# Optimization experiments

Measured on AMD Instinct MI355X. Metric: run time of the kernel, lower is better.

The kernel has to match this reference:

```python
import jax, jax.numpy as jnp
import numpy as np
from math import sqrt

V, D, H, HD, L, F, P, NL = 32000, 768, 12, 64, 12, 3072, 2048, 2
B, S = 8, 1024
EPS = 1e-5


def setup_inputs() -> dict:
    key = jax.random.key(0)
    ks = jax.random.split(key, 12)
    n = lambda k, sh: (jax.random.normal(k, sh, jnp.float32) * 0.02)
    return {
        'tokens': jax.random.randint(ks[0], (B, S), 0, V, dtype=jnp.int32),
        'tok_emb': n(ks[1], (V, D)),
        'pos_emb': n(ks[2], (P, D)),
        'emb_ln_s': jnp.ones((D,), jnp.float32), 'emb_ln_b': jnp.zeros((D,), jnp.float32),
        'Wq': n(ks[3], (L, H, D, HD)), 'bq': jnp.zeros((L, H, HD), jnp.float32),
        'Wk': n(ks[4], (L, H, D, HD)), 'bk': jnp.zeros((L, H, HD), jnp.float32),
        'Wv': n(ks[5], (L, H, D, HD)), 'bv': jnp.zeros((L, H, HD), jnp.float32),
        'Wo': n(ks[6], (L, D, D)), 'bo': jnp.zeros((L, D), jnp.float32),
        'ln1_s': jnp.ones((L, D), jnp.float32), 'ln1_b': jnp.zeros((L, D), jnp.float32),
        'ln2_s': jnp.ones((L, D), jnp.float32), 'ln2_b': jnp.zeros((L, D), jnp.float32),
        'W1': n(ks[7], (L, D, F)), 'b1': jnp.zeros((L, F), jnp.float32),
        'W2': n(ks[8], (L, F, D)), 'b2': jnp.zeros((L, D), jnp.float32),
        'Wc': n(ks[9], (D, NL)), 'bc': jnp.zeros((NL,), jnp.float32),
    }


def _ln(x, s, b):
    m = jnp.mean(x, -1, keepdims=True)
    v = jnp.mean((x - m) ** 2, -1, keepdims=True)
    return (x - m) * jax.lax.rsqrt(v + EPS) * s + b


def reference(tokens, tok_emb, pos_emb, emb_ln_s, emb_ln_b,
              Wq, bq, Wk, bk, Wv, bv, Wo, bo,
              ln1_s, ln1_b, ln2_s, ln2_b, W1, b1, W2, b2, Wc, bc):
    b, s = tokens.shape
    # embeddings (dropout is eval-mode identity)
    x = tok_emb[tokens] + pos_emb[:s][None, :, :]          # [b, s, D]
    x = _ln(x, emb_ln_s, emb_ln_b)
    scale = 1.0 / sqrt(HD)
    for l in range(L):
        xn = _ln(x, ln1_s[l], ln1_b[l])
        q = jnp.einsum('bsd,hdk->bhsk', xn, Wq[l]) + bq[l][:, None, :]
        k = jnp.einsum('bsd,hdk->bhsk', xn, Wk[l]) + bk[l][:, None, :]
        v = jnp.einsum('bsd,hdk->bhsk', xn, Wv[l]) + bv[l][:, None, :]
        scores = jnp.einsum('bhsk,bhtk->bhst', q, k) * scale   # [b,H,s,s]
        w = jax.nn.softmax(scores, axis=-1)
        o = jnp.einsum('bhst,bhtk->bhsk', w, v)                # [b,H,s,HD]
        o = o.transpose(0, 2, 1, 3).reshape(b, s, D)           # concat heads
        x = x + o @ Wo[l] + bo[l]
        xn = _ln(x, ln2_s[l], ln2_b[l])
        h = jax.nn.gelu(xn @ W1[l] + b1[l], approximate=False)
        x = x + h @ W2[l] + b2[l]
    # CLS token -> classifier (dropout identity)
    return x[:, 0, :] @ Wc + bc                                # [b, NL]
```

## Files before the change

kernel.cpp:

```cpp
#include <hip/hip_runtime.h>
#include <hip/hip_bf16.h>
#include <math.h>

#define B_   8
#define S_   1024
#define D_   768
#define H_   12
#define HD_  64
#define L_   12
#define F_   3072
#define NTOK 8192

typedef __bf16 bf16x8 __attribute__((ext_vector_type(8)));
typedef float  f32x4  __attribute__((ext_vector_type(4)));
typedef unsigned short u16;

static __device__ __forceinline__ unsigned short f2bf_bits(float f) {
    __hip_bfloat16 h = __float2bfloat16(f);
    return __builtin_bit_cast(unsigned short, h);
}
static __device__ __forceinline__ float bf2f(unsigned short u) {
    unsigned int t = ((unsigned int)u) << 16;
    return __builtin_bit_cast(float, t);
}
static __device__ __forceinline__ void gload16(const void* g, void* l) {
    __builtin_amdgcn_global_load_lds(
        (__attribute__((address_space(1))) void*)g,
        (__attribute__((address_space(3))) void*)l, 16, 0, 0);
}

__global__ __launch_bounds__(256)
void prep_layer_kernel(const float* __restrict__ Wq, const float* __restrict__ Wk,
                       const float* __restrict__ Wv, const float* __restrict__ Wo,
                       const float* __restrict__ W1, const float* __restrict__ W2,
                       int l, __hip_bfloat16* __restrict__ wbuf)
{
    const int id = blockIdx.x;
    const float* src; __hip_bfloat16* dst;
    int R, C, r0, c0;
    if (id < 432) {
        int dtile = id % 12, t = id / 12;
        int which = t / 12, h = t % 12;
        src = (which == 0 ? Wq : which == 1 ? Wk : Wv) + (size_t)(l*12 + h) * 768 * 64;
        dst = wbuf + (size_t)(which*768 + h*64) * 768;
        R = 768; C = 64; r0 = dtile * 64; c0 = 0;
    } else if (id < 576) {
        int t = id - 432;
        src = Wo + (size_t)l * 768 * 768;
        dst = wbuf + 1769472;
        R = 768; C = 768; r0 = (t / 12) * 64; c0 = (t % 12) * 64;
    } else if (id < 1152) {
        int t = id - 576;
        src = W1 + (size_t)l * 768 * 3072;
        dst = wbuf + 2359296;
        R = 768; C = 3072; r0 = (t % 12) * 64; c0 = (t / 12) * 64;
    } else {
        int t = id - 1152;
        src = W2 + (size_t)l * 3072 * 768;
        dst = wbuf + 4718592;
        R = 3072; C = 768; r0 = (t / 12) * 64; c0 = (t % 12) * 64;
    }
    __shared__ float tile[64][65];
    for (int i = threadIdx.x; i < 4096; i += 256) {
        int rr = i >> 6, cc = i & 63;
        tile[rr][cc] = src[(size_t)(r0 + rr) * C + (c0 + cc)];
    }
    __syncthreads();
    for (int i = threadIdx.x; i < 4096; i += 256) {
        int cc = i >> 6, rr = i & 63;
        dst[(size_t)(c0 + cc) * R + (r0 + rr)] = __float2bfloat16(tile[rr][cc]);
    }
}

__global__ __launch_bounds__(256)
void prep_bqkv_kernel(const float* __restrict__ bq, const float* __restrict__ bk,
                      const float* __restrict__ bv, float* __restrict__ bqkv)
{
    int i = blockIdx.x * 256 + threadIdx.x;
    int l = i / 2304, c = i % 2304;
    int which = c / 768, hk = c % 768;
    const float* src = which == 0 ? bq : which == 1 ? bk : bv;
    bqkv[i] = src[l*768 + hk];
}

__global__ __launch_bounds__(256)
void embed_ln_kernel(const int* __restrict__ tokens, const float* __restrict__ tok_emb,
                     const float* __restrict__ pos_emb, const float* __restrict__ gam,
                     const float* __restrict__ bet, float* __restrict__ x)
{
    const int row  = blockIdx.x*4 + (threadIdx.x >> 6);
    const int lane = threadIdx.x & 63;
    const int s    = row & (S_-1);
    const int tok  = tokens[row];
    const float* te = tok_emb + (size_t)tok * D_;
    const float* pe = pos_emb + (size_t)s   * D_;
    float v[12]; float s1 = 0.f, s2 = 0.f;
#pragma unroll
    for (int c = 0; c < 3; ++c) {
        const int base = c*256 + lane*4;
        float4 a = *(const float4*)(te + base);
        float4 p = *(const float4*)(pe + base);
        float t0 = a.x+p.x, t1 = a.y+p.y, t2 = a.z+p.z, t3 = a.w+p.w;
        v[c*4+0]=t0; v[c*4+1]=t1; v[c*4+2]=t2; v[c*4+3]=t3;
        s1 += t0+t1+t2+t3;
        s2 += t0*t0 + t1*t1 + t2*t2 + t3*t3;
    }
#pragma unroll
    for (int off = 32; off > 0; off >>= 1) { s1 += __shfl_xor(s1, off); s2 += __shfl_xor(s2, off); }
    const float mean = s1 * (1.f/768.f);
    const float rstd = rsqrtf(s2*(1.f/768.f) - mean*mean + 1e-5f);
    float* xr = x + (size_t)row * D_;
#pragma unroll
    for (int c = 0; c < 3; ++c) {
        const int base = c*256 + lane*4;
        float4 g = *(const float4*)(gam + base);
        float4 bb = *(const float4*)(bet + base);
        float4 o;
        o.x = (v[c*4+0]-mean)*rstd*g.x + bb.x;
        o.y = (v[c*4+1]-mean)*rstd*g.y + bb.y;
        o.z = (v[c*4+2]-mean)*rstd*g.z + bb.z;
        o.w = (v[c*4+3]-mean)*rstd*g.w + bb.w;
        *(float4*)(xr + base) = o;
    }
}

__global__ __launch_bounds__(256)
void ln_kernel(const float* __restrict__ xin, const float* __restrict__ gam,
               const float* __restrict__ bet, __hip_bfloat16* __restrict__ out)
{
    const int row  = blockIdx.x*4 + (threadIdx.x >> 6);
    const int lane = threadIdx.x & 63;
    const float* xr = xin + (size_t)row * D_;
    float v[12]; float s1 = 0.f, s2 = 0.f;
#pragma unroll
    for (int c = 0; c < 3; ++c) {
        float4 t = *(const float4*)(xr + c*256 + lane*4);
        v[c*4+0]=t.x; v[c*4+1]=t.y; v[c*4+2]=t.z; v[c*4+3]=t.w;
        s1 += t.x+t.y+t.z+t.w;
        s2 += t.x*t.x + t.y*t.y + t.z*t.z + t.w*t.w;
    }
#pragma unroll
    for (int off = 32; off > 0; off >>= 1) { s1 += __shfl_xor(s1, off); s2 += __shfl_xor(s2, off); }
    const float mean = s1 * (1.f/768.f);
    const float rstd = rsqrtf(s2*(1.f/768.f) - mean*mean + 1e-5f);
    unsigned short* op = (unsigned short*)out + (size_t)row * D_;
#pragma unroll
    for (int c = 0; c < 3; ++c) {
        const int base = c*256 + lane*4;
        float4 g = *(const float4*)(gam + base);
        float4 bb = *(const float4*)(bet + base);
        ushort4 pk;
        pk.x = f2bf_bits((v[c*4+0]-mean)*rstd*g.x + bb.x);
        pk.y = f2bf_bits((v[c*4+1]-mean)*rstd*g.y + bb.y);
        pk.z = f2bf_bits((v[c*4+2]-mean)*rstd*g.z + bb.z);
        pk.w = f2bf_bits((v[c*4+3]-mean)*rstd*g.w + bb.w);
        *(ushort4*)(op + base) = pk;
    }
}

template<int EPI>
__global__ __launch_bounds__(256)
void gemm_kernel(const __hip_bfloat16* __restrict__ A,
                 const __hip_bfloat16* __restrict__ Bt,
                 const float* __restrict__ bias,
                 __hip_bfloat16* __restrict__ outb,
                 __hip_bfloat16* __restrict__ outv,
                 int N, int K, int nTiles)
{
    __shared__ __hip_bfloat16 As[128*64];
    __shared__ __hip_bfloat16 Bs[128*64];

    const int tid  = threadIdx.x;
    const int lane = tid & 63;
    const int wid  = tid >> 6;

    const int nwg   = gridDim.x;
    const int chunk = nwg >> 3;
    const int bid   = blockIdx.x;
    const int swz   = (bid & 7) * chunk + (bid >> 3);
    const int m0 = (swz / nTiles) * 128;
    const int n0 = (swz % nTiles) * 128;

    const int srow = wid*32 + (lane >> 3);
    const int scol = ((lane & 7) ^ (srow & 7)) * 8;
    const __hip_bfloat16* aSrc = A  + (size_t)(m0 + srow) * K + scol;
    const __hip_bfloat16* bSrc = Bt + (size_t)(n0 + srow) * K + scol;
    char* aDst = (char*)As + wid*4096 + lane*16;
    char* bDst = (char*)Bs + wid*4096 + lane*16;

    f32x4 acc[4][4] = {};
    const int wm = wid >> 1, wn = wid & 1;
    const int cl = lane & 15, hi = lane >> 4;

    for (int kt = 0; kt < K; kt += 64) {
        __syncthreads();
#pragma unroll
        for (int i = 0; i < 4; ++i)
            gload16(aSrc + kt + (size_t)i*8*K, aDst + i*1024);
#pragma unroll
        for (int i = 0; i < 4; ++i)
            gload16(bSrc + kt + (size_t)i*8*K, bDst + i*1024);
        __syncthreads();

#pragma unroll
        for (int kk = 0; kk < 2; ++kk) {
            bf16x8 af[4], bfr[4];
#pragma unroll
            for (int m = 0; m < 4; ++m) {
                int row  = wm*64 + m*16 + cl;
                int slot = ((kk<<2) + hi) ^ (row & 7);
                af[m] = *(const bf16x8*)((const char*)As + row*128 + slot*16);
            }
#pragma unroll
            for (int n = 0; n < 4; ++n) {
                int row  = wn*64 + n*16 + cl;
                int slot = ((kk<<2) + hi) ^ (row & 7);
                bfr[n] = *(const bf16x8*)((const char*)Bs + row*128 + slot*16);
            }
#pragma unroll
            for (int m = 0; m < 4; ++m)
#pragma unroll
                for (int n = 0; n < 4; ++n)
                    acc[m][n] = __builtin_amdgcn_mfma_f32_16x16x32_bf16(af[m], bfr[n], acc[m][n], 0, 0, 0);
        }
    }

    const int rowBase = m0 + wm*64;
    const int colBase = n0 + wn*64;

    if constexpr (EPI == 0) {
        if (n0 < 1536) {
#pragma unroll
            for (int n = 0; n < 4; ++n) {
                const int col = colBase + n*16 + cl;
                const float bv = bias[col];
#pragma unroll
                for (int m = 0; m < 4; ++m) {
#pragma unroll
                    for (int i = 0; i < 4; ++i) {
                        const int row = rowBase + m*16 + hi*4 + i;
                        outb[(size_t)row*1536 + col] = __float2bfloat16(acc[m][n][i] + bv);
                    }
                }
            }
        } else {
#pragma unroll
            for (int n = 0; n < 4; ++n) {
                const int col = colBase + n*16 + cl;
                const float bv = bias[col];
                const int hd = col - 1536;
#pragma unroll
                for (int m = 0; m < 4; ++m) {
#pragma unroll
                    for (int i = 0; i < 4; ++i) {
                        const int row = rowBase + m*16 + hi*4 + i;
                        outv[(size_t)row*768 + hd] = __float2bfloat16(acc[m][n][i] + bv);
                    }
                }
            }
        }
    } else {
#pragma unroll
        for (int n = 0; n < 4; ++n) {
            const int col = colBase + n*16 + cl;
            const float bv = bias[col];
#pragma unroll
            for (int m = 0; m < 4; ++m) {
#pragma unroll
                for (int i = 0; i < 4; ++i) {
                    const int row = rowBase + m*16 + hi*4 + i;
                    const float v = acc[m][n][i] + bv;
                    const float y = 0.7978845608f * (v + 0.044715f*v*v*v);
                    const float e = __expf(-2.0f * fabsf(y));
                    const float th = (1.0f - e) / (1.0f + e);
                    const float g = 0.5f * v * (1.0f + copysignf(th, y));
                    outb[(size_t)row*N + col] = __float2bfloat16(g);
                }
            }
        }
    }
}

__global__ __launch_bounds__(256)
void gemm64_res_kernel(const __hip_bfloat16* __restrict__ A,
                       const __hip_bfloat16* __restrict__ Bt,
                       const float* __restrict__ bias,
                       float* __restrict__ outf,
                       int N, int K, int nTiles)
{
    __shared__ __hip_bfloat16 As[64*64];
    __shared__ __hip_bfloat16 Bs[128*64];

    const int tid  = threadIdx.x;
    const int lane = tid & 63;
    const int wid  = tid >> 6;

    const int nwg   = gridDim.x;
    const int chunk = nwg >> 3;
    const int bid   = blockIdx.x;
    const int swz   = (bid & 7) * chunk + (bid >> 3);
    const int m0 = (swz / nTiles) * 64;
    const int n0 = (swz % nTiles) * 128;

    const int lrow = lane >> 3;
    const int scol = ((lane & 7) ^ lrow) * 8;
    const __hip_bfloat16* aSrc = A  + (size_t)(m0 + wid*16 + lrow) * K + scol;
    const __hip_bfloat16* bSrc = Bt + (size_t)(n0 + wid*32 + lrow) * K + scol;
    char* aDst = (char*)As + wid*2048 + lane*16;
    char* bDst = (char*)Bs + wid*4096 + lane*16;

    f32x4 acc[2][4] = {};
    const int wm = wid >> 1, wn = wid & 1;
    const int cl = lane & 15, hi = lane >> 4;

    for (int kt = 0; kt < K; kt += 64) {
        __syncthreads();
#pragma unroll
        for (int i = 0; i < 2; ++i)
            gload16(aSrc + kt + (size_t)i*8*K, aDst + i*1024);
#pragma unroll
        for (int i = 0; i < 4; ++i)
            gload16(bSrc + kt + (size_t)i*8*K, bDst + i*1024);
        __syncthreads();

#pragma unroll
        for (int kk = 0; kk < 2; ++kk) {
            bf16x8 af[2], bfr[4];
#pragma unroll
            for (int m = 0; m < 2; ++m) {
                int row  = wm*32 + m*16 + cl;
                int slot = ((kk<<2) + hi) ^ (row & 7);
                af[m] = *(const bf16x8*)((const char*)As + row*128 + slot*16);
            }
#pragma unroll
            for (int n = 0; n < 4; ++n) {
                int row  = wn*64 + n*16 + cl;
                int slot = ((kk<<2) + hi) ^ (row & 7);
                bfr[n] = *(const bf16x8*)((const char*)Bs + row*128 + slot*16);
            }
#pragma unroll
            for (int m = 0; m < 2; ++m)
#pragma unroll
                for (int n = 0; n < 4; ++n)
                    acc[m][n] = __builtin_amdgcn_mfma_f32_16x16x32_bf16(af[m], bfr[n], acc[m][n], 0, 0, 0);
        }
    }

    const int rowBase = m0 + wm*32;
    const int colBase = n0 + wn*64;
#pragma unroll
    for (int n = 0; n < 4; ++n) {
        const int col = colBase + n*16 + cl;
        const float bv = bias[col];
#pragma unroll
        for (int m = 0; m < 2; ++m) {
#pragma unroll
            for (int i = 0; i < 4; ++i) {
                const int row = rowBase + m*16 + hi*4 + i;
                outf[(size_t)row*N + col] += acc[m][n][i] + bv;
            }
        }
    }
}

__global__ __launch_bounds__(256)
void vtrans_kernel(const __hip_bfloat16* __restrict__ vp, __hip_bfloat16* __restrict__ vT)
{
    __shared__ u16 tile[64][65];
    const int id = blockIdx.x;
    const int b = id / 192, r = id % 192;
    const int hdt = r / 16, st = r % 16;
    const u16* src = (const u16*)vp + ((size_t)(b*1024 + st*64))*768 + hdt*64;
    u16* dst = (u16*)vT + ((size_t)(b*768 + hdt*64))*1024 + st*64;
    for (int i = threadIdx.x; i < 4096; i += 256) {
        int rr = i >> 6, cc = i & 63;
        tile[rr][cc] = src[(size_t)rr*768 + cc];
    }
    __syncthreads();
    for (int i = threadIdx.x; i < 4096; i += 256) {
        int cc = i >> 6, rr = i & 63;
        dst[(size_t)cc*1024 + rr] = tile[rr][cc];
    }
}

__global__ __launch_bounds__(256)
void attn_kernel(const __hip_bfloat16* __restrict__ qkb, const __hip_bfloat16* __restrict__ vtb,
                 __hip_bfloat16* __restrict__ attno)
{
    __shared__ __align__(16) char Ks[2][8192];
    __shared__ __align__(16) char Vs[2][8192];
    __shared__ __align__(16) char Ps[8192];

    const u16* qk = (const u16*)qkb;
    const u16* vt = (const u16*)vtb;
    const int nwg = gridDim.x, bid = blockIdx.x, chunk = nwg >> 3;
    const int swz = (bid & 7) * chunk + (bid >> 3);
    const int bh = swz >> 4, qb = swz & 15;
    const int b = bh / H_, h = bh % H_;
    const int tid = threadIdx.x;
    const int lane = tid & 63, wid = tid >> 6;
    const int cl = lane & 15, hi = lane >> 4;
    const size_t browq = (size_t)(b*S_ + qb*64);

    bf16x8 qf[2];
    {
        const u16* qp = qk + (browq + wid*16 + cl)*1536 + h*64;
        qf[0] = *(const bf16x8*)(qp + hi*8);
        qf[1] = *(const bf16x8*)(qp + 32 + hi*8);
    }

    const int lrow = lane >> 3;
    const int scol = ((lane & 7) ^ lrow) * 8;
    const u16* kbase = qk + ((size_t)b*S_ + wid*16 + lrow)*1536 + 768 + h*64 + scol;
    const u16* vbase = vt + (((size_t)(b*H_ + h))*64 + wid*16 + lrow)*1024 + scol;
    const int ldst = wid*2048 + lane*16;

    f32x4 acc_o[4] = {};
    float m_run = -1e30f;
    float l_part[4] = {0.f, 0.f, 0.f, 0.f};
    char* pbase = Ps + wid*2048;

    {
        gload16(kbase,                  Ks[0] + ldst);
        gload16(kbase + (size_t)8*1536, Ks[0] + ldst + 1024);
        gload16(vbase,                  Vs[0] + ldst);
        gload16(vbase + 8*1024,         Vs[0] + ldst + 1024);
    }

    for (int t = 0; t < 16; ++t) {
        __syncthreads();
        if (t < 15) {
            const int nb = (t+1) & 1;
            const u16* kn = kbase + (size_t)(t+1)*64*1536;
            const u16* vn = vbase + (t+1)*64;
            gload16(kn,                  Ks[nb] + ldst);
            gload16(kn + (size_t)8*1536, Ks[nb] + ldst + 1024);
            gload16(vn,                  Vs[nb] + ldst);
            gload16(vn + 8*1024,         Vs[nb] + ldst + 1024);
        }
        const char* ks = Ks[t & 1];
        const char* vs = Vs[t & 1];

        f32x4 sc[4] = {};
#pragma unroll
        for (int kk = 0; kk < 2; ++kk) {
            bf16x8 kf[4];
#pragma unroll
            for (int n = 0; n < 4; ++n) {
                const int row = n*16 + cl;
                kf[n] = *(const bf16x8*)(ks + row*128 + (((kk*4 + hi) ^ (cl & 7)) << 4));
            }
#pragma unroll
            for (int n = 0; n < 4; ++n)
                sc[n] = __builtin_amdgcn_mfma_f32_16x16x32_bf16(qf[kk], kf[n], sc[n], 0, 0, 0);
        }

#pragma unroll
        for (int n = 0; n < 4; ++n)
#pragma unroll
            for (int i = 0; i < 4; ++i)
                sc[n][i] *= 0.125f;

        float gmax = sc[0][0];
#pragma unroll
        for (int n = 0; n < 4; ++n)
#pragma unroll
            for (int i = 0; i < 4; ++i)
                gmax = fmaxf(gmax, sc[n][i]);
        gmax = fmaxf(gmax, __shfl_xor(gmax, 1));
        gmax = fmaxf(gmax, __shfl_xor(gmax, 2));
        gmax = fmaxf(gmax, __shfl_xor(gmax, 4));
        gmax = fmaxf(gmax, __shfl_xor(gmax, 8));
        if (gmax > m_run + 4.0f) {
            const float corr = __expf(m_run - gmax);
            m_run = gmax;
#pragma unroll
            for (int i = 0; i < 4; ++i) l_part[i] *= corr;
#pragma unroll
            for (int nd = 0; nd < 4; ++nd)
#pragma unroll
                for (int i = 0; i < 4; ++i)
                    acc_o[nd][i] *= corr;
        }

#pragma unroll
        for (int n = 0; n < 4; ++n) {
#pragma unroll
            for (int i = 0; i < 4; ++i) {
                const float e = __expf(sc[n][i] - m_run);
                l_part[i] += e;
                const int q = hi*4 + i;
                const int slot = (n*2 + (cl >> 3)) ^ (q & 7);
                *(u16*)(pbase + q*128 + slot*16 + (cl & 7)*2) = f2bf_bits(e);
            }
        }

        asm volatile("s_waitcnt lgkmcnt(0)" ::: "memory");
        __builtin_amdgcn_sched_barrier(0);

#pragma unroll
        for (int kk = 0; kk < 2; ++kk) {
            const bf16x8 pf = *(const bf16x8*)(pbase + cl*128 + (((kk*4 + hi) ^ (cl & 7)) << 4));
            bf16x8 vf[4];
#pragma unroll
            for (int nd = 0; nd < 4; ++nd) {
                const int d = nd*16 + cl;
                vf[nd] = *(const bf16x8*)(vs + d*128 + (((kk*4 + hi) ^ (d & 7)) << 4));
            }
#pragma unroll
            for (int nd = 0; nd < 4; ++nd)
                acc_o[nd] = __builtin_amdgcn_mfma_f32_16x16x32_bf16(pf, vf[nd], acc_o[nd], 0, 0, 0);
        }
    }

    u16* op = (u16*)attno;
#pragma unroll
    for (int i = 0; i < 4; ++i) {
        float l = l_part[i];
        l += __shfl_xor(l, 1);
        l += __shfl_xor(l, 2);
        l += __shfl_xor(l, 4);
        l += __shfl_xor(l, 8);
        const float inv = 1.f / l;
        const size_t row = browq + wid*16 + hi*4 + i;
#pragma unroll
        for (int nd = 0; nd < 4; ++nd)
            op[row*768 + h*64 + nd*16 + cl] = f2bf_bits(acc_o[nd][i] * inv);
    }
}

__global__ __launch_bounds__(256)
void cls_kernel(const float* __restrict__ x, const float* __restrict__ Wc,
                const float* __restrict__ bc, float* __restrict__ out)
{
    const int b = blockIdx.x;
    const float* xr = x + (size_t)b * S_ * D_;
    float a0 = 0.f, a1 = 0.f;
    for (int d = threadIdx.x; d < 768; d += 256) {
        float xv = xr[d];
        a0 += xv * Wc[d*2+0];
        a1 += xv * Wc[d*2+1];
    }
#pragma unroll
    for (int off = 32; off > 0; off >>= 1) { a0 += __shfl_xor(a0, off); a1 += __shfl_xor(a1, off); }
    __shared__ float r0[4], r1[4];
    const int w = threadIdx.x >> 6;
    if ((threadIdx.x & 63) == 0) { r0[w] = a0; r1[w] = a1; }
    __syncthreads();
    if (threadIdx.x == 0) {
        out[b*2+0] = r0[0]+r0[1]+r0[2]+r0[3] + bc[0];
        out[b*2+1] = r1[0]+r1[1]+r1[2]+r1[3] + bc[1];
    }
}

extern "C" void kernel_launch(void* const* d_in, const int* in_sizes, int n_in,
                              void* d_out, int out_size, void* d_ws, size_t ws_size,
                              hipStream_t stream)
{
    const int*   tokens  = (const int*)  d_in[0];
    const float* tok_emb = (const float*)d_in[1];
    const float* pos_emb = (const float*)d_in[2];
    const float* e_s     = (const float*)d_in[3];
    const float* e_b     = (const float*)d_in[4];
    const float* Wq      = (const float*)d_in[5];
    const float* bq      = (const float*)d_in[6];
    const float* Wk      = (const float*)d_in[7];
    const float* bk      = (const float*)d_in[8];
    const float* Wv      = (const float*)d_in[9];
    const float* bv      = (const float*)d_in[10];
    const float* Wo      = (const float*)d_in[11];
    const float* bo      = (const float*)d_in[12];
    const float* l1s     = (const float*)d_in[13];
    const float* l1b     = (const float*)d_in[14];
    const float* l2s     = (const float*)d_in[15];
    const float* l2b     = (const float*)d_in[16];
    const float* W1      = (const float*)d_in[17];
    const float* b1      = (const float*)d_in[18];
    const float* W2      = (const float*)d_in[19];
    const float* b2      = (const float*)d_in[20];
    const float* Wc      = (const float*)d_in[21];
    const float* bc      = (const float*)d_in[22];
    (void)in_sizes; (void)n_in; (void)out_size;

    if (ws_size < 102346752) return;

    char* ws = (char*)d_ws;
    __hip_bfloat16* wbuf = (__hip_bfloat16*)(ws + 0);
    float*          bqkv = (float*)(ws + 14155776);
    float*          x    = (float*)(ws + 14266368);
    __hip_bfloat16* xn   = (__hip_bfloat16*)(ws + 39432192);
    __hip_bfloat16* qk   = (__hip_bfloat16*)(ws + 52015104);
    __hip_bfloat16* vT   = (__hip_bfloat16*)(ws + 77180928);
    __hip_bfloat16* att  = (__hip_bfloat16*)(ws + 89763840);
    __hip_bfloat16* vpl  = att;
    __hip_bfloat16* hbuf = qk;

    __hip_bfloat16* wqkv_t = wbuf;
    __hip_bfloat16* wo_t   = wbuf + 1769472;
    __hip_bfloat16* w1_t   = wbuf + 2359296;
    __hip_bfloat16* w2_t   = wbuf + 4718592;

    prep_bqkv_kernel<<<108, 256, 0, stream>>>(bq, bk, bv, bqkv);
    embed_ln_kernel<<<2048, 256, 0, stream>>>(tokens, tok_emb, pos_emb, e_s, e_b, x);

    for (int l = 0; l < L_; ++l) {
        prep_layer_kernel<<<1728, 256, 0, stream>>>(Wq, Wk, Wv, Wo, W1, W2, l, wbuf);
        ln_kernel<<<2048, 256, 0, stream>>>(x, l1s + l*768, l1b + l*768, xn);
        gemm_kernel<0><<<1152, 256, 0, stream>>>(xn, wqkv_t, bqkv + l*2304, qk, vpl, 2304, 768, 18);
        vtrans_kernel<<<1536, 256, 0, stream>>>(vpl, vT);
        attn_kernel<<<1536, 256, 0, stream>>>(qk, vT, att);
        gemm64_res_kernel<<<768, 256, 0, stream>>>(att, wo_t, bo + l*768, x, 768, 768, 6);
        ln_kernel<<<2048, 256, 0, stream>>>(x, l2s + l*768, l2b + l*768, xn);
        gemm_kernel<1><<<1536, 256, 0, stream>>>(xn, w1_t, b1 + l*3072, hbuf, nullptr, 3072, 768, 24);
        gemm64_res_kernel<<<768, 256, 0, stream>>>(hbuf, w2_t, b2 + l*768, x, 768, 3072, 6);
    }
    cls_kernel<<<8, 256, 0, stream>>>(x, Wc, bc, (float*)d_out);
}
```

Before: 3.363 ms.

## Fuse V transpose into QKV GEMM epilogue and enlarge attention blocks

The QKV GEMM epilogue now transposes the V tile through swizzled shared memory and writes it straight into the transposed V layout. This removes the separate vtrans kernel and its extra global round trip. The attention kernel now runs 512 threads (8 waves) per block, covering 128 queries. Each K/V tile is therefore loaded once for twice as many queries, with half the grid and one global load per thread per buffer. The cost is a larger P scratch buffer and extra barriers in the GEMM epilogue.

```diff
diff --git a/kernel.cpp b/kernel.cpp
--- a/kernel.cpp
+++ b/kernel.cpp
@@ -167,8 +167,9 @@
                  __hip_bfloat16* __restrict__ outv,
                  int N, int K, int nTiles)
 {
-    __shared__ __hip_bfloat16 As[128*64];
-    __shared__ __hip_bfloat16 Bs[128*64];
+    __shared__ __align__(16) char smem[32768];
+    __hip_bfloat16* As = (__hip_bfloat16*)smem;
+    __hip_bfloat16* Bs = (__hip_bfloat16*)(smem + 16384);
 
     const int tid  = threadIdx.x;
     const int lane = tid & 63;
@@ -244,19 +245,33 @@
                 }
             }
         } else {
+            __syncthreads();
 #pragma unroll
             for (int n = 0; n < 4; ++n) {
                 const int col = colBase + n*16 + cl;
                 const float bv = bias[col];
-                const int hd = col - 1536;
+                const int hdl = wn*64 + n*16 + cl;
 #pragma unroll
                 for (int m = 0; m < 4; ++m) {
-#pragma unroll
-                    for (int i = 0; i < 4; ++i) {
-                        const int row = rowBase + m*16 + hi*4 + i;
-                        outv[(size_t)row*768 + hd] = __float2bfloat16(acc[m][n][i] + bv);
-                    }
+                    const int sl = wm*64 + m*16 + hi*4;
+                    ushort4 pk;
+                    pk.x = f2bf_bits(acc[m][n][0] + bv);
+                    pk.y = f2bf_bits(acc[m][n][1] + bv);
+                    pk.z = f2bf_bits(acc[m][n][2] + bv);
+                    pk.w = f2bf_bits(acc[m][n][3] + bv);
+                    *(ushort4*)(smem + hdl*256 + ((((sl >> 3) ^ (hdl & 15))) << 4) + (sl & 7)*2) = pk;
                 }
+            }
+            __syncthreads();
+            const int hdl2 = tid >> 1;
+            const int sh   = (tid & 1) * 64;
+            const int hdg  = (n0 - 1536) + hdl2;
+            const int bb   = m0 >> 10;
+            u16* dst = (u16*)outv + ((size_t)(bb*768) + hdg)*1024 + (m0 & 1023) + sh;
+#pragma unroll
+            for (int j = 0; j < 8; ++j) {
+                const int slot = ((sh >> 3) + j) ^ (hdl2 & 15);
+                *(float4*)((char*)dst + j*16) = *(const float4*)(smem + hdl2*256 + (slot << 4));
             }
         }
     } else {
@@ -363,44 +378,24 @@
     }
 }
 
-__global__ __launch_bounds__(256)
-void vtrans_kernel(const __hip_bfloat16* __restrict__ vp, __hip_bfloat16* __restrict__ vT)
-{
-    __shared__ u16 tile[64][65];
-    const int id = blockIdx.x;
-    const int b = id / 192, r = id % 192;
-    const int hdt = r / 16, st = r % 16;
-    const u16* src = (const u16*)vp + ((size_t)(b*1024 + st*64))*768 + hdt*64;
-    u16* dst = (u16*)vT + ((size_t)(b*768 + hdt*64))*1024 + st*64;
-    for (int i = threadIdx.x; i < 4096; i += 256) {
-        int rr = i >> 6, cc = i & 63;
-        tile[rr][cc] = src[(size_t)rr*768 + cc];
-    }
-    __syncthreads();
-    for (int i = threadIdx.x; i < 4096; i += 256) {
-        int cc = i >> 6, rr = i & 63;
-        dst[(size_t)cc*1024 + rr] = tile[rr][cc];
-    }
-}
-
-__global__ __launch_bounds__(256)
+__global__ __launch_bounds__(512)
 void attn_kernel(const __hip_bfloat16* __restrict__ qkb, const __hip_bfloat16* __restrict__ vtb,
                  __hip_bfloat16* __restrict__ attno)
 {
     __shared__ __align__(16) char Ks[2][8192];
     __shared__ __align__(16) char Vs[2][8192];
-    __shared__ __align__(16) char Ps[8192];
+    __shared__ __align__(16) char Ps[16384];
 
     const u16* qk = (const u16*)qkb;
     const u16* vt = (const u16*)vtb;
     const int nwg = gridDim.x, bid = blockIdx.x, chunk = nwg >> 3;
     const int swz = (bid & 7) * chunk + (bid >> 3);
-    const int bh = swz >> 4, qb = swz & 15;
+    const int bh = swz >> 3, qb = swz & 7;
     const int b = bh / H_, h = bh % H_;
     const int tid = threadIdx.x;
     const int lane = tid & 63, wid = tid >> 6;
     const int cl = lane & 15, hi = lane >> 4;
-    const size_t browq = (size_t)(b*S_ + qb*64);
+    const size_t browq = (size_t)(b*S_ + qb*128);
 
     bf16x8 qf[2];
     {
@@ -411,9 +406,9 @@
 
     const int lrow = lane >> 3;
     const int scol = ((lane & 7) ^ lrow) * 8;
-    const u16* kbase = qk + ((size_t)b*S_ + wid*16 + lrow)*1536 + 768 + h*64 + scol;
-    const u16* vbase = vt + (((size_t)(b*H_ + h))*64 + wid*16 + lrow)*1024 + scol;
-    const int ldst = wid*2048 + lane*16;
+    const u16* kbase = qk + ((size_t)b*S_ + wid*8 + lrow)*1536 + 768 + h*64 + scol;
+    const u16* vbase = vt + (((size_t)(b*H_ + h))*64 + wid*8 + lrow)*1024 + scol;
+    const int ldst = wid*1024 + lane*16;
 
     f32x4 acc_o[4] = {};
     float m_run = -1e30f;
@@ -421,22 +416,16 @@
     char* pbase = Ps + wid*2048;
 
     {
-        gload16(kbase,                  Ks[0] + ldst);
-        gload16(kbase + (size_t)8*1536, Ks[0] + ldst + 1024);
-        gload16(vbase,                  Vs[0] + ldst);
-        gload16(vbase + 8*1024,         Vs[0] + ldst + 1024);
+        gload16(kbase, Ks[0] + ldst);
+        gload16(vbase, Vs[0] + ldst);
     }
 
     for (int t = 0; t < 16; ++t) {
         __syncthreads();
         if (t < 15) {
             const int nb = (t+1) & 1;
-            const u16* kn = kbase + (size_t)(t+1)*64*1536;
-            const u16* vn = vbase + (t+1)*64;
-            gload16(kn,                  Ks[nb] + ldst);
-            gload16(kn + (size_t)8*1536, Ks[nb] + ldst + 1024);
-            gload16(vn,                  Vs[nb] + ldst);
-            gload16(vn + 8*1024,         Vs[nb] + ldst + 1024);
+            gload16(kbase + (size_t)(t+1)*64*1536, Ks[nb] + ldst);
+            gload16(vbase + (t+1)*64,              Vs[nb] + ldst);
         }
         const char* ks = Ks[t & 1];
         const char* vs = Vs[t & 1];
@@ -592,7 +581,6 @@
     __hip_bfloat16* qk   = (__hip_bfloat16*)(ws + 52015104);
     __hip_bfloat16* vT   = (__hip_bfloat16*)(ws + 77180928);
     __hip_bfloat16* att  = (__hip_bfloat16*)(ws + 89763840);
-    __hip_bfloat16* vpl  = att;
     __hip_bfloat16* hbuf = qk;
 
     __hip_bfloat16* wqkv_t = wbuf;
@@ -606,9 +594,8 @@
     for (int l = 0; l < L_; ++l) {
         prep_layer_kernel<<<1728, 256, 0, stream>>>(Wq, Wk, Wv, Wo, W1, W2, l, wbuf);
         ln_kernel<<<2048, 256, 0, stream>>>(x, l1s + l*768, l1b + l*768, xn);
-        gemm_kernel<0><<<1152, 256, 0, stream>>>(xn, wqkv_t, bqkv + l*2304, qk, vpl, 2304, 768, 18);
-        vtrans_kernel<<<1536, 256, 0, stream>>>(vpl, vT);
-        attn_kernel<<<1536, 256, 0, stream>>>(qk, vT, att);
+        gemm_kernel<0><<<1152, 256, 0, stream>>>(xn, wqkv_t, bqkv + l*2304, qk, vT, 2304, 768, 18);
+        attn_kernel<<<768, 512, 0, stream>>>(qk, vT, att);
         gemm64_res_kernel<<<768, 256, 0, stream>>>(att, wo_t, bo + l*768, x, 768, 768, 6);
         ln_kernel<<<2048, 256, 0, stream>>>(x, l2s + l*768, l2b + l*768, xn);
         gemm_kernel<1><<<1536, 256, 0, stream>>>(xn, w1_t, b1 + l*3072, hbuf, nullptr, 3072, 768, 24);
```

Result: faster. 3.241 ms (-3.6%).
